# Kernel tuning notes

Hardware: AMD Instinct MI355X
Metric: run time of the kernel (lower is better)

## Reference

```python
import jax, jax.numpy as jnp
import numpy as np

B, T, D = 256, 500, 3   # batch, time steps, input features (time, mag, err)
U, C = 512, 10          # PhasedLSTM units, n_classes
R_ON = 0.05             # open ratio of the phased time gate
ALPHA = 1e-3            # leak rate during closed phase
LN_EPS = 1e-3           # keras LayerNormalization default epsilon


def _glorot(key, shape):
    lim = np.sqrt(6.0 / (shape[0] + shape[1])).astype(np.float32)
    return jax.random.uniform(key, shape, jnp.float32, -lim, lim)


def setup_inputs() -> dict:
    key = jax.random.key(0)
    ks = jax.random.split(key, 12)
    x = jax.random.normal(ks[0], (B, T, D), jnp.float32)
    # monotonically increasing observation times per sample
    times = jnp.cumsum(jax.random.uniform(ks[1], (B, T), jnp.float32), axis=1)
    # layer 0 PhasedLSTM params (gate order i, f, g, o)
    W0 = _glorot(ks[2], (D, 4 * U)); R0 = _glorot(ks[3], (U, 4 * U)); b0 = jnp.zeros((4 * U,), jnp.float32)
    tau0 = jnp.exp(jax.random.uniform(ks[4], (U,), jnp.float32, 0.0, 3.0))
    s0 = jax.random.uniform(ks[5], (U,), jnp.float32) * tau0
    # layer 1
    W1 = _glorot(ks[6], (U, 4 * U)); R1 = _glorot(ks[7], (U, 4 * U)); b1 = jnp.zeros((4 * U,), jnp.float32)
    tau1 = jnp.exp(jax.random.uniform(ks[8], (U,), jnp.float32, 0.0, 3.0))
    s1 = jax.random.uniform(ks[9], (U,), jnp.float32) * tau1
    # per-layer LayerNorm params
    g0 = jnp.ones((U,), jnp.float32); be0 = jnp.zeros((U,), jnp.float32)
    g1 = jnp.ones((U,), jnp.float32); be1 = jnp.zeros((U,), jnp.float32)
    # classifier head
    Wf = _glorot(ks[10], (U, C)); bf = jnp.zeros((C,), jnp.float32)
    return dict(x=x, times=times, W0=W0, R0=R0, b0=b0, tau0=tau0, s0=s0, g0=g0, be0=be0,
                W1=W1, R1=R1, b1=b1, tau1=tau1, s1=s1, g1=g1, be1=be1, Wf=Wf, bf=bf)


def _layernorm(h, g, b):
    m = jnp.mean(h, axis=-1, keepdims=True)
    v = jnp.var(h, axis=-1, keepdims=True)
    return (h - m) * jax.lax.rsqrt(v + LN_EPS) * g + b


def _time_gate(t, tau, s):
    # t: [B], tau/s: [U] -> k: [B, U]
    phi = jnp.mod(t[:, None] - s, tau) / tau
    return jnp.where(phi < 0.5 * R_ON, 2.0 * phi / R_ON,
                     jnp.where(phi < R_ON, 2.0 - 2.0 * phi / R_ON, ALPHA * phi))


def _plstm_step(xi, ti, h, c, W, R, b, tau, s):
    z = xi @ W + h @ R + b                       # [B, 4U]
    i, f, g, o = jnp.split(z, 4, axis=-1)
    i = jax.nn.sigmoid(i); f = jax.nn.sigmoid(f); o = jax.nn.sigmoid(o)
    c_new = f * c + i * jnp.tanh(g)
    h_new = o * jnp.tanh(c_new)
    k = _time_gate(ti, tau, s)                   # phased time gate
    return k * h_new + (1.0 - k) * h, k * c_new + (1.0 - k) * c


def reference(x, times, W0, R0, b0, tau0, s0, g0, be0,
              W1, R1, b1, tau1, s1, g1, be1, Wf, bf):
    xt = jnp.transpose(x, (1, 0, 2))  # [T, B, D]
    tt = times.T                      # [T, B]
    zeros = jnp.zeros((x.shape[0], U), x.dtype)
    init = (zeros, zeros, zeros, zeros)

    def step(carry, inp):
        h0, c0, h1, c1 = carry
        xi, ti = inp
        h0n, c0n = _plstm_step(xi, ti, h0, c0, W0, R0, b0, tau0, s0)
        a0 = _layernorm(h0n, g0, be0)   # normed output feeds next layer; raw state is carried
        h1n, c1n = _plstm_step(a0, ti, h1, c1, W1, R1, b1, tau1, s1)
        a1 = _layernorm(h1n, g1, be1)
        probs = jax.nn.softmax(a1 @ Wf + bf)  # dropout is identity at inference
        return (h0n, c0n, h1n, c1n), probs

    _, out = jax.lax.scan(step, init, (xt, tt))  # out: [T, B, C]
    return jnp.transpose(out, (1, 0, 2))
```

## Files before the change

kernel.cpp:

```cpp
#include <hip/hip_runtime.h>
#include <hip/hip_bf16.h>


#define NB 256
#define NTHR 384
#define T_STEPS 500
#define RON 0.05f
#define ALPHA_LEAK 1e-3f

typedef short short8 __attribute__((ext_vector_type(8)));
typedef float f32x4 __attribute__((ext_vector_type(4)));
typedef unsigned long long ull;

#define OFF_WSWZ 0u
#define OFF_U1   6291456u
#define OFF_V1   6299648u
#define OFF_WFP  6307840u
#define OFF_UFV  6328320u
#define OFF_H0B  6328448u
#define OFF_H1B  6852736u
#define OFF_ST0  7377024u
#define OFF_ST1  7508096u
#define OFF_FLG0 7639168u
#define OFF_FLG1 7640192u
#define ZERO_BYTES 1312768u

#define SMEM_BYTES 156160

#define AT_LD(p)    __hip_atomic_load((p), __ATOMIC_RELAXED, __HIP_MEMORY_SCOPE_AGENT)
#define AT_ST(p, v) __hip_atomic_store((p), (v), __ATOMIC_RELAXED, __HIP_MEMORY_SCOPE_AGENT)

__device__ __forceinline__ short f2bf(float x) {
  unsigned u = __float_as_uint(x);
  unsigned r = (u + 0x7fffu + ((u >> 16) & 1u)) >> 16;
  return (short)r;
}
__device__ __forceinline__ float bf2f(short s) {
  return __uint_as_float(((unsigned)(unsigned short)s) << 16);
}
__device__ __forceinline__ float sigm(float x) { return 1.f / (1.f + __expf(-x)); }
__device__ __forceinline__ float tanh_f(float x) {
  float cx = fminf(fmaxf(x, -15.f), 15.f);
  float e = __expf(2.f * cx);
  return (e - 1.f) / (e + 1.f);
}
__device__ __forceinline__ float timegate(float t, float tau, float s) {
  float phi = fmodf(t - s, tau);
  if (phi < 0.f) phi += tau;
  phi /= tau;
  return phi < 0.5f * RON ? (2.f / RON) * phi
       : (phi < RON ? 2.f - (2.f / RON) * phi : ALPHA_LEAK * phi);
}
__device__ __forceinline__ int fragidx(int m, int k) {
  return ((((k >> 5) * 2 + (m >> 4)) * 64) + (((k >> 3) & 3) * 16) + (m & 15)) * 8 + (k & 7);
}

__global__ void prep_weights(const float* __restrict__ R0, const float* __restrict__ W1,
                             const float* __restrict__ R1, const float* __restrict__ g0,
                             short* __restrict__ Wswz) {
  int t = blockIdx.x * 256 + threadIdx.x;
  int lane = t & 63; int rest = t >> 6;
  int nf = rest & 1;  rest >>= 1;
  int kb = rest & 15; rest >>= 4;
  int ch = rest & 1;  rest >>= 1;
  int mm = rest % 3;  int slice = rest / 3;
  int c = ch * 32 + nf * 16 + (lane & 15);
  int gate = c >> 4;
  int unit = slice * 16 + (c & 15);
  int gcol = gate * 512 + unit;
  int k0 = kb * 32 + (lane >> 4) * 8;
  const float* src = (mm == 0) ? R0 : (mm == 1 ? W1 : R1);
  short8 o;
  #pragma unroll
  for (int e = 0; e < 8; ++e) {
    float v = src[(size_t)(k0 + e) * 2048 + gcol];
    if (mm == 1) v *= g0[k0 + e];
    o[e] = f2bf(v);
  }
  *(short8*)(Wswz + (size_t)t * 8) = o;
}

__global__ void prep_vecs(const float* __restrict__ W1, const float* __restrict__ g0,
                          const float* __restrict__ be0,
                          float* __restrict__ u1, float* __restrict__ v1) {
  int c = blockIdx.x * 256 + threadIdx.x;
  float su = 0.f, sv = 0.f;
  for (int k = 0; k < 512; ++k) {
    float w = W1[(size_t)k * 2048 + c];
    su += be0[k] * w; sv += g0[k] * w;
  }
  u1[c] = su; v1[c] = sv;
}

__global__ void prep_head(const float* __restrict__ Wf, const float* __restrict__ g1,
                          const float* __restrict__ be1, const float* __restrict__ bfv,
                          float* __restrict__ Wfp, float* __restrict__ ufv) {
  int t = blockIdx.x * 256 + threadIdx.x;
  if (t < 5120) {
    int kk = t / 640, rem = t - kk * 640, c = rem >> 6, l = rem & 63;
    int k = 8 * l + kk;
    Wfp[t] = g1[k] * Wf[k * 10 + c];
  }
  if (t < 10) {
    float su = bfv[t], sv = 0.f;
    for (int k = 0; k < 512; ++k) {
      float w = Wf[k * 10 + t];
      su += be1[k] * w; sv += g1[k] * w;
    }
    ufv[t] = su; ufv[16 + t] = sv;
  }
}

struct Ptrs {
  const float *x, *times, *W0, *b0, *tau0, *s0, *b1, *tau1, *s1;
  const float *u1v, *v1v, *Wfp, *ufv;
  short *H0b, *H1b;
  float *St0, *St1;
  unsigned *flag0, *flag1;
  float *out;
};

__launch_bounds__(NTHR, 1)
__global__ void plstm_persist(Ptrs P, const short* __restrict__ Wswz) {
  extern __shared__ char smem[];
  short* h0b  = (short*)smem;
  short* h1bL = (short*)(smem + 32768);
  float* h0f  = (float*)(smem + 98304);
  float* c0f = h0f + 512;
  float* h1f = h0f + 1024;
  float* c1f = h0f + 1536;
  float* mu0 = (float*)(smem + 106496); float* rs0 = mu0 + 32;
  float* mu1 = mu0 + 64;                float* rs1 = mu0 + 96;
  float* zbv = (float*)(smem + 107008);
  float* prm = (float*)(smem + 132736);
  float* wfl = (float*)(smem + 134784);
  float* ufl = (float*)(smem + 155264);
  float* xtb = (float*)(smem + 155392);
  float* xtb1 = (float*)(smem + 155904);

  const int tid = threadIdx.x;
  const int g = blockIdx.x & 7;
  const int slice = blockIdx.x >> 3;
  const int wid = tid >> 6, lane = tid & 63;
  const int mm = wid >> 1, ch = wid & 1;
  const int gm0 = g * 32;

  for (int i = tid; i < 2048; i += NTHR) h0f[i] = 0.f;
  for (int i = tid; i < 512; i += NTHR) {
    float v;
    if (i < 192)      { int f = i >> 6, c = i & 63; v = P.W0[f * 2048 + ((c >> 4) << 9) + slice * 16 + (c & 15)]; }
    else if (i < 256) { int c = i & 63; v = P.b0[((c >> 4) << 9) + slice * 16 + (c & 15)]; }
    else if (i < 320) { int c = i & 63; int gc = ((c >> 4) << 9) + slice * 16 + (c & 15);
                        v = P.b1[gc] + P.u1v[gc]; }
    else if (i < 384) { int c = i & 63; v = P.v1v[((c >> 4) << 9) + slice * 16 + (c & 15)]; }
    else if (i < 448) v = 0.f;
    else if (i < 464) v = P.tau0[slice * 16 + (i & 15)];
    else if (i < 480) v = P.s0[slice * 16 + (i & 15)];
    else if (i < 496) v = P.tau1[slice * 16 + (i & 15)];
    else              v = P.s1[slice * 16 + (i & 15)];
    prm[i] = v;
  }
  for (int i = tid; i < 5120; i += NTHR) wfl[i] = P.Wfp[i];
  if (tid < 32) ufl[tid] = P.ufv[tid];

  short8 wr[16][2];
  {
    const short* wb = Wswz + ((((size_t)slice * 3 + mm) * 2 + ch) * 32 * 64) * 8;
    #pragma unroll
    for (int kb = 0; kb < 16; ++kb)
      #pragma unroll
      for (int nf = 0; nf < 2; ++nf) {
        wr[kb][nf] = *(const short8*)(wb + ((kb * 2 + nf) * 64 + lane) * 8);
        asm volatile("" : "+v"(wr[kb][nf]));
      }
  }
  __syncthreads();

  for (int r = 0; r < T_STEPS + 2; ++r) {
    const int bufA = (r + 1) & 1;
    const int bufB = r & 1;
    short* h1s = h1bL + bufB * 16384;

    if (wid == 0) {
      int m = lane & 31;
      if (lane < 32) {
        int step = (r < T_STEPS) ? r : (T_STEPS - 1);
        const float* xp = P.x + ((size_t)(gm0 + m) * T_STEPS + step) * 3;
        xtb[m * 4 + 0] = xp[0];
        xtb[m * 4 + 1] = xp[1];
        xtb[m * 4 + 2] = xp[2];
        xtb[m * 4 + 3] = P.times[(size_t)(gm0 + m) * T_STEPS + step];
      } else {
        int s1_ = (r >= 1) ? (r - 1) : 0;
        xtb1[m] = P.times[(size_t)(gm0 + m) * T_STEPS + s1_];
      }
      const unsigned tgt = (lane < 32) ? (unsigned)((r <= T_STEPS) ? r : 0)
                                       : (unsigned)((r >= 2) ? r : 0);
      const unsigned* fp = (lane < 32) ? (P.flag0 + g * 32 + m)
                                       : (P.flag1 + g * 32 + m);
      for (int it_ = 0; it_ < 100000; ++it_) {
        unsigned v = AT_LD(fp);
        if (__all((int)(v >= tgt))) break;
      }
    }
    __syncthreads();

    if (tid < 320) {
      const ull* srcA = (const ull*)(P.H0b + ((size_t)bufA * 8 + g) * 16384);
      const ull* srcB = (const ull*)(P.H1b + ((size_t)bufB * 8 + g) * 16384);
      ull* dA = (ull*)h0b;
      ull* dB = (ull*)h1s;
      #pragma unroll
      for (int half = 0; half < 2; ++half) {
        ull tmp[13];
        const int idx0 = tid + half * 13 * 320;
        #pragma unroll
        for (int k = 0; k < 13; ++k) {
          int idx = idx0 + k * 320;
          if (idx < 8192) tmp[k] = AT_LD(idx < 4096 ? &srcA[idx] : &srcB[idx - 4096]);
        }
        #pragma unroll
        for (int k = 0; k < 13; ++k) {
          int idx = idx0 + k * 320;
          if (idx < 8192) { if (idx < 4096) dA[idx] = tmp[k]; else dB[idx - 4096] = tmp[k]; }
        }
      }
    } else {
      const int layer = lane >> 5, m = lane & 31;
      const float* base = layer ? (P.St1 + ((size_t)bufB * 8 + g) * 2048 + m * 64)
                                : (P.St0 + ((size_t)bufA * 8 + g) * 2048 + m * 64);
      const ull* bu = (const ull*)base;
      float s_ = 0.f, q_ = 0.f;
      #pragma unroll
      for (int sl = 0; sl < 32; ++sl) {
        ull v = AT_LD(bu + sl);
        s_ += __uint_as_float((unsigned)v);
        q_ += __uint_as_float((unsigned)(v >> 32));
      }
      float mu = s_ * (1.f / 512.f);
      float var = q_ * (1.f / 512.f) - mu * mu;
      float rs = rsqrtf(var + 1e-3f);
      if (layer == 0) { mu0[m] = mu; rs0[m] = rs; }
      else            { mu1[m] = mu; rs1[m] = rs; }
    }
    __syncthreads();
    float m1r = 0.f, r1r = 0.f;
    if (wid == 1) { m1r = mu1[slice]; r1r = rs1[slice]; }

    {
      f32x4 acc[2][2] = {};
      const short* asrc = (mm == 2) ? h1s : h0b;
      #pragma unroll
      for (int kb = 0; kb < 16; ++kb) {
        short8 a0 = *(const short8*)(asrc + ((kb * 2 + 0) * 64 + lane) * 8);
        short8 a1 = *(const short8*)(asrc + ((kb * 2 + 1) * 64 + lane) * 8);
        #pragma unroll
        for (int nf = 0; nf < 2; ++nf) {
          acc[0][nf] = __builtin_amdgcn_mfma_f32_16x16x32_bf16(a0, wr[kb][nf], acc[0][nf], 0, 0, 0);
          acc[1][nf] = __builtin_amdgcn_mfma_f32_16x16x32_bf16(a1, wr[kb][nf], acc[1][nf], 0, 0, 0);
        }
      }
      float* z = zbv + mm * 2144;
      #pragma unroll
      for (int mf = 0; mf < 2; ++mf)
        #pragma unroll
        for (int nf = 0; nf < 2; ++nf)
          #pragma unroll
          for (int q = 0; q < 4; ++q) {
            int row = mf * 16 + (lane >> 4) * 4 + q;
            int col = ch * 32 + nf * 16 + (lane & 15);
            z[row * 67 + col] = acc[mf][nf][q];
          }
    }
    __syncthreads();

    const bool l0act = (r < T_STEPS);
    const bool l1act = (r >= 1 && r <= T_STEPS);
    if (tid < 256 && l0act) {
      int m = tid >> 3, u0 = (tid & 7) << 1;
      float x0 = xtb[m * 4 + 0], x1 = xtb[m * 4 + 1], x2 = xtb[m * 4 + 2];
      float tmv = xtb[m * 4 + 3];
      unsigned pack = 0;
      float hnv[2];
      #pragma unroll
      for (int uu = 0; uu < 2; ++uu) {
        int u = u0 + uu, id = m * 16 + u;
        float zg4[4];
        #pragma unroll
        for (int q = 0; q < 4; ++q) {
          int c = q * 16 + u;
          zg4[q] = zbv[m * 67 + c] + prm[192 + c]
                 + x0 * prm[c] + x1 * prm[64 + c] + x2 * prm[128 + c];
        }
        float iv = sigm(zg4[0]), fv = sigm(zg4[1]), gv = tanh_f(zg4[2]), ov = sigm(zg4[3]);
        float cold = c0f[id], hold = h0f[id];
        float cp = fv * cold + iv * gv;
        float hp = ov * tanh_f(cp);
        float k = timegate(tmv, prm[448 + u], prm[464 + u]);
        float hn = k * hp + (1.f - k) * hold;
        float cn = k * cp + (1.f - k) * cold;
        h0f[id] = hn; c0f[id] = cn; hnv[uu] = hn;
        pack |= ((unsigned)(unsigned short)f2bf(hn)) << (16 * uu);
      }
      AT_ST((unsigned*)(P.H0b + ((size_t)bufB * 8 + g) * 16384 + fragidx(m, slice * 16 + u0)), pack);
      float sr = hnv[0] + hnv[1], qr = hnv[0] * hnv[0] + hnv[1] * hnv[1];
      sr += __shfl_down(sr, 4, 8); qr += __shfl_down(qr, 4, 8);
      sr += __shfl_down(sr, 2, 8); qr += __shfl_down(qr, 2, 8);
      sr += __shfl_down(sr, 1, 8); qr += __shfl_down(qr, 1, 8);
      if ((tid & 7) == 0) {
        ull pv = ((ull)__float_as_uint(qr) << 32) | __float_as_uint(sr);
        AT_ST((ull*)(P.St0 + ((size_t)bufB * 8 + g) * 2048) + m * 32 + slice, pv);
      }
    }
    #pragma unroll
    for (int pass = 0; pass < 2; ++pass) {
      int idx = -1;
      if (pass == 0 && tid >= 256) idx = tid - 256;
      if (pass == 1 && tid < 128)  idx = 128 + tid;
      if (idx >= 0 && l1act) {
        int m = idx >> 3, u0 = (idx & 7) << 1;
        float mu0m = mu0[m], rs0m = rs0[m];
        float tmv = xtb1[m];
        unsigned pack = 0;
        float hnv[2];
        #pragma unroll
        for (int uu = 0; uu < 2; ++uu) {
          int u = u0 + uu, id = m * 16 + u;
          float zg4[4];
          #pragma unroll
          for (int q = 0; q < 4; ++q) {
            int c = q * 16 + u;
            float zA = zbv[2144 + m * 67 + c];
            float zB = zbv[4288 + m * 67 + c];
            zg4[q] = rs0m * zA + zB + prm[256 + c] - mu0m * rs0m * prm[320 + c];
          }
          float iv = sigm(zg4[0]), fv = sigm(zg4[1]), gv = tanh_f(zg4[2]), ov = sigm(zg4[3]);
          float cold = c1f[id], hold = h1f[id];
          float cp = fv * cold + iv * gv;
          float hp = ov * tanh_f(cp);
          float k = timegate(tmv, prm[480 + u], prm[496 + u]);
          float hn = k * hp + (1.f - k) * hold;
          float cn = k * cp + (1.f - k) * cold;
          h1f[id] = hn; c1f[id] = cn; hnv[uu] = hn;
          pack |= ((unsigned)(unsigned short)f2bf(hn)) << (16 * uu);
        }
        AT_ST((unsigned*)(P.H1b + ((size_t)bufA * 8 + g) * 16384 + fragidx(m, slice * 16 + u0)), pack);
        float sr = hnv[0] + hnv[1], qr = hnv[0] * hnv[0] + hnv[1] * hnv[1];
        sr += __shfl_down(sr, 4, 8); qr += __shfl_down(qr, 4, 8);
        sr += __shfl_down(sr, 2, 8); qr += __shfl_down(qr, 2, 8);
        sr += __shfl_down(sr, 1, 8); qr += __shfl_down(qr, 1, 8);
        if ((idx & 7) == 0) {
          ull pv = ((ull)__float_as_uint(qr) << 32) | __float_as_uint(sr);
          AT_ST((ull*)(P.St1 + ((size_t)bufA * 8 + g) * 2048) + m * 32 + slice, pv);
        }
      }
    }
    __syncthreads();

    if (tid == 0) {
      if (l0act) AT_ST(P.flag0 + g * 32 + slice, (unsigned)(r + 1));
      if (l1act) AT_ST(P.flag1 + g * 32 + slice, (unsigned)(r + 1));
    }
    if (wid == 1 && r >= 2) {
      int msam = slice;
      short8 hv8 = *(const short8*)(h1s + fragidx(msam, lane * 8));
      float lg[10];
      #pragma unroll
      for (int c = 0; c < 10; ++c) lg[c] = 0.f;
      #pragma unroll
      for (int kk = 0; kk < 8; ++kk) {
        float hv = bf2f(hv8[kk]);
        const float* wf = wfl + kk * 640 + lane;
        #pragma unroll
        for (int c = 0; c < 10; ++c) lg[c] += hv * wf[c * 64];
      }
      #pragma unroll
      for (int off = 32; off > 0; off >>= 1)
        #pragma unroll
        for (int c = 0; c < 10; ++c) lg[c] += __shfl_down(lg[c], off, 64);
      if (lane == 0) {
        float logit[10], mx = -1e30f;
        #pragma unroll
        for (int c = 0; c < 10; ++c) {
          logit[c] = r1r * lg[c] + ufl[c] - m1r * r1r * ufl[16 + c];
          mx = fmaxf(mx, logit[c]);
        }
        float ssum = 0.f;
        #pragma unroll
        for (int c = 0; c < 10; ++c) { logit[c] = expf(logit[c] - mx); ssum += logit[c]; }
        float inv = 1.f / ssum;
        float* op = P.out + ((size_t)(gm0 + msam) * T_STEPS + (r - 2)) * 10;
        #pragma unroll
        for (int c = 0; c < 10; ++c) op[c] = logit[c] * inv;
      }
    }
  }
}

extern "C" void kernel_launch(void* const* d_in, const int* in_sizes, int n_in,
                              void* d_out, int out_size, void* d_ws, size_t ws_size,
                              hipStream_t stream) {
  const float* x    = (const float*)d_in[0];
  const float* tms  = (const float*)d_in[1];
  const float* W0   = (const float*)d_in[2];
  const float* R0   = (const float*)d_in[3];
  const float* b0   = (const float*)d_in[4];
  const float* tau0 = (const float*)d_in[5];
  const float* s0   = (const float*)d_in[6];
  const float* g0   = (const float*)d_in[7];
  const float* be0  = (const float*)d_in[8];
  const float* W1   = (const float*)d_in[9];
  const float* R1   = (const float*)d_in[10];
  const float* b1   = (const float*)d_in[11];
  const float* tau1 = (const float*)d_in[12];
  const float* s1   = (const float*)d_in[13];
  const float* g1   = (const float*)d_in[14];
  const float* be1  = (const float*)d_in[15];
  const float* Wf   = (const float*)d_in[16];
  const float* bfv  = (const float*)d_in[17];

  char* ws = (char*)d_ws;
  short* Wswz = (short*)(ws + OFF_WSWZ);
  float* u1m  = (float*)(ws + OFF_U1);
  float* v1m  = (float*)(ws + OFF_V1);
  float* Wfpm = (float*)(ws + OFF_WFP);
  float* ufvm = (float*)(ws + OFF_UFV);

  Ptrs P;
  P.x = x; P.times = tms; P.W0 = W0; P.b0 = b0; P.tau0 = tau0; P.s0 = s0;
  P.b1 = b1; P.tau1 = tau1; P.s1 = s1;
  P.u1v = u1m; P.v1v = v1m; P.Wfp = Wfpm; P.ufv = ufvm;
  P.H0b = (short*)(ws + OFF_H0B);
  P.H1b = (short*)(ws + OFF_H1B);
  P.St0 = (float*)(ws + OFF_ST0);
  P.St1 = (float*)(ws + OFF_ST1);
  P.flag0 = (unsigned*)(ws + OFF_FLG0);
  P.flag1 = (unsigned*)(ws + OFF_FLG1);
  P.out = (float*)d_out;

  hipFuncSetAttribute(reinterpret_cast<const void*>(plstm_persist),
                      hipFuncAttributeMaxDynamicSharedMemorySize, SMEM_BYTES);

  prep_weights<<<1536, 256, 0, stream>>>(R0, W1, R1, g0, Wswz);
  prep_vecs<<<8, 256, 0, stream>>>(W1, g0, be0, u1m, v1m);
  prep_head<<<20, 256, 0, stream>>>(Wf, g1, be1, bfv, Wfpm, ufvm);
  hipMemsetAsync(ws + OFF_H0B, 0, ZERO_BYTES, stream);
  plstm_persist<<<NB, NTHR, SMEM_BYTES, stream>>>(P, Wswz);
}
```

Measured before the change: 5.326 ms.

## Merge layer flags, split polling wave, use direct global-to-LDS loads

Collapses the two per-layer ready flags into one flag per slice that covers both layers. Polling moves to a dedicated wave with s_sleep backoff, and the x/time loads move to a separate wave. The hidden-state exchange now uses global_load_lds (16 bytes per lane) straight into shared memory instead of loading relaxed atomics into registers and then storing to LDS. The direct loads may not be coherent with the other blocks' atomic stores and nothing waits on vmcnt, so stale or late data is possible. Relying on one flag for both layers also changes the ordering guarantees.

```diff
diff --git a/kernel.cpp b/kernel.cpp
--- a/kernel.cpp
+++ b/kernel.cpp
@@ -29,6 +29,11 @@
 
 #define AT_LD(p)    __hip_atomic_load((p), __ATOMIC_RELAXED, __HIP_MEMORY_SCOPE_AGENT)
 #define AT_ST(p, v) __hip_atomic_store((p), (v), __ATOMIC_RELAXED, __HIP_MEMORY_SCOPE_AGENT)
+
+#define G2L(gp, lp) \
+  __builtin_amdgcn_global_load_lds( \
+      (const __attribute__((address_space(1))) void*)(gp), \
+      (__attribute__((address_space(3))) void*)(lp), 16, 0, 16)
 
 __device__ __forceinline__ short f2bf(float x) {
   unsigned u = __float_as_uint(x);
@@ -182,6 +187,14 @@
     short* h1s = h1bL + bufB * 16384;
 
     if (wid == 0) {
+      const unsigned tgt = (unsigned)r;
+      const unsigned* fp = P.flag0 + g * 32 + (lane & 31);
+      for (int it_ = 0; it_ < 100000; ++it_) {
+        unsigned v = (lane < 32) ? AT_LD(fp) : 0xFFFFFFFFu;
+        if (__all((int)(v >= tgt))) break;
+        __builtin_amdgcn_s_sleep(1);
+      }
+    } else if (wid == 4) {
       int m = lane & 31;
       if (lane < 32) {
         int step = (r < T_STEPS) ? r : (T_STEPS - 1);
@@ -194,38 +207,21 @@
         int s1_ = (r >= 1) ? (r - 1) : 0;
         xtb1[m] = P.times[(size_t)(gm0 + m) * T_STEPS + s1_];
       }
-      const unsigned tgt = (lane < 32) ? (unsigned)((r <= T_STEPS) ? r : 0)
-                                       : (unsigned)((r >= 2) ? r : 0);
-      const unsigned* fp = (lane < 32) ? (P.flag0 + g * 32 + m)
-                                       : (P.flag1 + g * 32 + m);
-      for (int it_ = 0; it_ < 100000; ++it_) {
-        unsigned v = AT_LD(fp);
-        if (__all((int)(v >= tgt))) break;
-      }
     }
     __syncthreads();
 
-    if (tid < 320) {
-      const ull* srcA = (const ull*)(P.H0b + ((size_t)bufA * 8 + g) * 16384);
-      const ull* srcB = (const ull*)(P.H1b + ((size_t)bufB * 8 + g) * 16384);
-      ull* dA = (ull*)h0b;
-      ull* dB = (ull*)h1s;
-      #pragma unroll
-      for (int half = 0; half < 2; ++half) {
-        ull tmp[13];
-        const int idx0 = tid + half * 13 * 320;
-        #pragma unroll
-        for (int k = 0; k < 13; ++k) {
-          int idx = idx0 + k * 320;
-          if (idx < 8192) tmp[k] = AT_LD(idx < 4096 ? &srcA[idx] : &srcB[idx - 4096]);
-        }
-        #pragma unroll
-        for (int k = 0; k < 13; ++k) {
-          int idx = idx0 + k * 320;
-          if (idx < 8192) { if (idx < 4096) dA[idx] = tmp[k]; else dB[idx - 4096] = tmp[k]; }
-        }
-      }
-    } else {
+    if (tid < 256) {
+      const char* gA = (const char*)(P.H0b + ((size_t)bufA * 8 + g) * 16384);
+      const char* gB = (const char*)(P.H1b + ((size_t)bufB * 8 + g) * 16384);
+      char* lA = (char*)h0b;
+      char* lB = (char*)h1s;
+      #pragma unroll
+      for (int k = 0; k < 8; ++k) {
+        size_t off = (size_t)(k * 256 + tid) * 16;
+        G2L(gA + off, lA + off);
+        G2L(gB + off, lB + off);
+      }
+    } else if (wid == 5) {
       const int layer = lane >> 5, m = lane & 31;
       const float* base = layer ? (P.St1 + ((size_t)bufB * 8 + g) * 2048 + m * 64)
                                 : (P.St0 + ((size_t)bufA * 8 + g) * 2048 + m * 64);
@@ -357,9 +353,8 @@
     }
     __syncthreads();
 
-    if (tid == 0) {
-      if (l0act) AT_ST(P.flag0 + g * 32 + slice, (unsigned)(r + 1));
-      if (l1act) AT_ST(P.flag1 + g * 32 + slice, (unsigned)(r + 1));
+    if (tid == 0 && r <= T_STEPS) {
+      AT_ST(P.flag0 + g * 32 + slice, (unsigned)(r + 1));
     }
     if (wid == 1 && r >= 2) {
       int msam = slice;
```

Result: no change. 5.245 ms (-1.5%).
